# Performance work log

Hardware: AMD Instinct MI355X
Metric: run time of the kernel (lower is better)

## Reference

```python
import jax, jax.numpy as jnp
import numpy as np

# Standard asymmetric NF4 value table (bitsandbytes / flute nf_utils, bits=4, symmetric=False)
NF4_VALUES = np.array([
    -1.0, -0.6961928009986877, -0.5250730514526367, -0.39491748809814453,
    -0.28444138169288635, -0.18477343022823334, -0.09105003625154495, 0.0,
    0.07958029955625534, 0.16093020141124725, 0.2461123913526535,
    0.33791524171829224, 0.44070982933044434, 0.5626170039176941,
    0.7229568362236023, 1.0], dtype=np.float32)
# Pivots are midpoints between consecutive values -> nearest-value bucketing via searchsorted
NF4_PIVOTS = (NF4_VALUES[:-1] + NF4_VALUES[1:]) / 2.0

GROUP_SIZE = 64
IN_FEATURES = 4096
OUT_FEATURES = 4096
BATCH, SEQ = 4, 2048


def setup_inputs() -> dict:
    key = jax.random.key(0)
    k1, k2 = jax.random.split(key)
    inp = jax.random.normal(k1, (BATCH, SEQ, IN_FEATURES), dtype=jnp.float32)
    weight = jax.random.normal(k2, (OUT_FEATURES, IN_FEATURES), dtype=jnp.float32) * 0.02
    # scales initialized exactly as in __init__: per-group absmax of the weight
    scales = jnp.max(jnp.abs(weight.reshape(-1, GROUP_SIZE)), axis=1, keepdims=True)  # [out*in/64, 1]
    return {
        "inp": inp,
        "weight": weight,
        "scales": scales,
        "values": jnp.asarray(NF4_VALUES),
        "pivots": jnp.asarray(NF4_PIVOTS),
    }


def _manual_nf4(weight, scales, values, pivots, group_size):
    # groupwise absmax-normalize, nearest-value lookup via pivot search, dequantize
    w = weight.reshape(-1, group_size)                 # [n_groups, group_size]
    scaled = jnp.clip(w / scales, -1.0, 1.0)
    idx = jnp.searchsorted(pivots, scaled)             # nearest NF4 code
    qweight = values[idx] * scales                     # dequantized bf16-style weight
    return qweight.reshape(weight.shape)


def reference(inp, weight, scales, values, pivots):
    qweight = _manual_nf4(weight, scales, values, pivots, GROUP_SIZE)  # [out, in]
    # F.linear(inp, qweight), bias=None
    return jnp.einsum('bsi,oi->bso', inp, qweight)
```

## Files before the change

kernel.cpp:

```cpp
#include <hip/hip_runtime.h>
#include <hip/hip_bf16.h>
#include <stdint.h>

#define M_DIM 8192
#define N_DIM 4096
#define K_DIM 4096
#define BM 256
#define BN 256
#define BK 64
#define NT (K_DIM / BK)

#define CVT_BLOCKS 8192
#define DQ_BLOCKS  4096

typedef float f32x16 __attribute__((ext_vector_type(16)));
typedef __bf16 bf16x8 __attribute__((ext_vector_type(8)));
typedef short s16x8 __attribute__((ext_vector_type(8)));

template <typename AB>
__device__ __forceinline__ auto mfma_32x32x16(AB a, AB b, f32x16 c, int)
    -> decltype(__builtin_amdgcn_mfma_f32_32x32x16_bf16(a, b, c, 0, 0, 0)) {
  return __builtin_amdgcn_mfma_f32_32x32x16_bf16(a, b, c, 0, 0, 0);
}
template <typename AB>
__device__ __forceinline__ f32x16 mfma_32x32x16(AB a, AB b, f32x16 c, long) {
  return __builtin_amdgcn_mfma_f32_32x32x16_bf16(
      __builtin_bit_cast(s16x8, a), __builtin_bit_cast(s16x8, b), c, 0, 0, 0);
}

__device__ __forceinline__ uint16_t f2b(float f) {
  union { float f; uint32_t u; } v; v.f = f;
  uint32_t u = v.u;
  u += 0x7FFFu + ((u >> 16) & 1u);
  return (uint16_t)(u >> 16);
}

__global__ __launch_bounds__(256) void prep(const float* __restrict__ inp,
                                            uint16_t* __restrict__ A_bf16,
                                            const float* __restrict__ w,
                                            const float* __restrict__ scales,
                                            const float* __restrict__ values,
                                            const float* __restrict__ pivots,
                                            uint16_t* __restrict__ B_bf16) {
  if (blockIdx.x < CVT_BLOCKS) {
    size_t t0 = (size_t)blockIdx.x * 256 + threadIdx.x;
    const float4* pin = (const float4*)inp;
    uint2* pout = (uint2*)A_bf16;
#pragma unroll
    for (int it = 0; it < 4; ++it) {
      size_t i = t0 + (size_t)it * ((size_t)CVT_BLOCKS * 256);
      float4 a = pin[i];
      uint2 o;
      o.x = (uint32_t)f2b(a.x) | ((uint32_t)f2b(a.y) << 16);
      o.y = (uint32_t)f2b(a.z) | ((uint32_t)f2b(a.w) << 16);
      pout[i] = o;
    }
  } else {
    __shared__ float sv[16];
    if (threadIdx.x < 16) sv[threadIdx.x] = values[threadIdx.x];
    float pv[15];
#pragma unroll
    for (int j = 0; j < 15; ++j) pv[j] = pivots[j];
    __syncthreads();
    size_t t0 = (size_t)(blockIdx.x - CVT_BLOCKS) * 256 + threadIdx.x;
    const float4* pw = (const float4*)w;
    uint2* pout = (uint2*)B_bf16;
#pragma unroll
    for (int it = 0; it < 4; ++it) {
      size_t i = t0 + (size_t)it * ((size_t)DQ_BLOCKS * 256);
      float scale = scales[i >> 4];
      float psc[15];
#pragma unroll
      for (int j = 0; j < 15; ++j) psc[j] = pv[j] * scale;
      float4 a = pw[i];
      float e[4] = {a.x, a.y, a.z, a.w};
      uint32_t hw[4];
#pragma unroll
      for (int k = 0; k < 4; ++k) {
        int idx = 0;
#pragma unroll
        for (int j = 0; j < 15; ++j) idx += (psc[j] < e[k]) ? 1 : 0;
        hw[k] = f2b(sv[idx] * scale);
      }
      uint2 o = {hw[0] | (hw[1] << 16), hw[2] | (hw[3] << 16)};
      pout[i] = o;
    }
  }
}


#define GLL(SRC, LOFF)                                                        \
  __builtin_amdgcn_global_load_lds(                                           \
      (__attribute__((address_space(1))) void*)(void*)(SRC),                  \
      (__attribute__((address_space(3))) void*)(smem + (LOFF)), 16, 0, 0)

#define STAGE_A(NB, KH, KEL)                                                  \
  do {                                                                        \
    GLL(Ab + gs0 + (KEL) + (KH) * 32, (NB) * 32768u + (KH) * 16384u + l0);    \
    GLL(Ab + gs1 + (KEL) + (KH) * 32, (NB) * 32768u + (KH) * 16384u + l1);    \
  } while (0)
#define STAGE_B(NB, KH, KEL)                                                  \
  do {                                                                        \
    GLL(Bb + gs0 + (KEL) + (KH) * 32,                                         \
        65536u + (NB) * 32768u + (KH) * 16384u + l0);                         \
    GLL(Bb + gs1 + (KEL) + (KH) * 32,                                         \
        65536u + (NB) * 32768u + (KH) * 16384u + l1);                         \
  } while (0)

#define LGKM6                                                                 \
  do {                                                                        \
    asm volatile("s_waitcnt lgkmcnt(6)" ::: "memory");                        \
    __builtin_amdgcn_sched_barrier(0);                                        \
  } while (0)
#define LGKM0                                                                 \
  do {                                                                        \
    asm volatile("s_waitcnt lgkmcnt(0)" ::: "memory");                        \
    __builtin_amdgcn_sched_barrier(0);                                        \
  } while (0)

#define READ6(A0, A1, A2, A3, B0, B1, CUR, KH, CB)                            \
  do {                                                                        \
    const uint32_t _ab = (CUR) * 32768u + (KH) * 16384u + aoff;               \
    const uint32_t _bb = 65536u + (CUR) * 32768u + (KH) * 16384u + boff;      \
    A0 = *(const bf16x8*)(smem + _ab + (CB));                                 \
    B0 = *(const bf16x8*)(smem + _bb + (CB));                                 \
    B1 = *(const bf16x8*)(smem + _bb + 2048u + (CB));                         \
    A1 = *(const bf16x8*)(smem + _ab + 2048u + (CB));                         \
    A2 = *(const bf16x8*)(smem + _ab + 4096u + (CB));                         \
    A3 = *(const bf16x8*)(smem + _ab + 6144u + (CB));                         \
  } while (0)

#define MM8(A0, A1, A2, A3, B0, B1)                                           \
  do {                                                                        \
    __builtin_amdgcn_s_setprio(1);                                            \
    acc[0][0] = mfma_32x32x16(A0, B0, acc[0][0], 0);                          \
    acc[0][1] = mfma_32x32x16(A0, B1, acc[0][1], 0);                          \
    acc[1][0] = mfma_32x32x16(A1, B0, acc[1][0], 0);                          \
    acc[1][1] = mfma_32x32x16(A1, B1, acc[1][1], 0);                          \
    acc[2][0] = mfma_32x32x16(A2, B0, acc[2][0], 0);                          \
    acc[2][1] = mfma_32x32x16(A2, B1, acc[2][1], 0);                          \
    acc[3][0] = mfma_32x32x16(A3, B0, acc[3][0], 0);                          \
    acc[3][1] = mfma_32x32x16(A3, B1, acc[3][1], 0);                          \
    __builtin_amdgcn_sched_barrier(0);                                        \
    __builtin_amdgcn_s_setprio(0);                                            \
  } while (0)

#define TILE(CUR, NB, KEL)                                                    \
  do {                                                                        \
    bf16x8 xa0, xa1, xa2, xa3, xb0, xb1;                                      \
    bf16x8 ya0, ya1, ya2, ya3, yb0, yb1;                                      \
    READ6(xa0, xa1, xa2, xa3, xb0, xb1, CUR, 0u, cb0);            \
    STAGE_A(NB, 0u, KEL);                                                     \
    STAGE_B(NB, 0u, KEL);                                                     \
    READ6(ya0, ya1, ya2, ya3, yb0, yb1, CUR, 0u, cb1);            \
    LGKM6;                                                 \
    MM8(xa0, xa1, xa2, xa3, xb0, xb1);                                        \
    READ6(xa0, xa1, xa2, xa3, xb0, xb1, CUR, 1u, cb0);            \
    STAGE_A(NB, 1u, KEL);                                                     \
    STAGE_B(NB, 1u, KEL);                                                     \
    LGKM6;                                                 \
    MM8(ya0, ya1, ya2, ya3, yb0, yb1);                                        \
    READ6(ya0, ya1, ya2, ya3, yb0, yb1, CUR, 1u, cb1);            \
    LGKM6;                                                 \
    MM8(xa0, xa1, xa2, xa3, xb0, xb1);                                        \
    LGKM0;                                                 \
    MM8(ya0, ya1, ya2, ya3, yb0, yb1);                                        \
    asm volatile("s_waitcnt vmcnt(0)" ::: "memory");  \
    __builtin_amdgcn_s_barrier();                                             \
    __builtin_amdgcn_sched_barrier(0);                                        \
  } while (0)

__global__ __launch_bounds__(512, 2) void gemm_bt(const uint16_t* __restrict__ A,
                                                  const uint16_t* __restrict__ B,
                                                  float* __restrict__ C) {
  __shared__ char smem[131072];
  const int tid = threadIdx.x;
  const int wave = tid >> 6;
  const int lane = tid & 63;

  const int bid = blockIdx.x;
  const int wg = (bid & 7) * 64 + (bid >> 3);
  const int bm = wg >> 4;
  const int bn = wg & 15;

  const int wm = wave >> 2;
  const int wn = wave & 3;
  const int r31 = lane & 31;
  const int hi = lane >> 5;

  const int swz = ((r31 >> 1) & 3) ^ ((r31 >> 3) & 1);
  const uint32_t cb0 = (uint32_t)(((hi ^ swz) * 16));
  const uint32_t cb1 = (uint32_t)((((2 + hi) ^ swz) * 16));
  const uint32_t aoff = (uint32_t)(wm * 8192 + r31 * 64);
  const uint32_t boff = (uint32_t)(wn * 4096 + r31 * 64);

  const int s0 = wave * 128 + lane;
  const int r0 = s0 >> 2;
  const uint32_t gs0 =
      (uint32_t)r0 * K_DIM +
      (uint32_t)((((s0 & 3) ^ (((r0 >> 1) & 3) ^ ((r0 >> 3) & 1))) * 8));
  const int s1 = s0 + 64;
  const int r1 = s1 >> 2;
  const uint32_t gs1 =
      (uint32_t)r1 * K_DIM +
      (uint32_t)((((s1 & 3) ^ (((r1 >> 1) & 3) ^ ((r1 >> 3) & 1))) * 8));
  const uint32_t l0 = (uint32_t)(wave * 2048);
  const uint32_t l1 = l0 + 1024u;

  const uint16_t* Ab = A + (size_t)bm * BM * K_DIM;
  const uint16_t* Bb = B + (size_t)bn * BN * K_DIM;

  f32x16 acc[4][2] = {};

  STAGE_A(0u, 0u, 0u);
  STAGE_B(0u, 0u, 0u);
  STAGE_A(0u, 1u, 0u);
  STAGE_B(0u, 1u, 0u);
  asm volatile("s_waitcnt vmcnt(0)" ::: "memory");
  __builtin_amdgcn_s_barrier();
  __builtin_amdgcn_sched_barrier(0);

  for (int kt = 0; kt < NT; kt += 2) {
    const uint32_t kel0 = (uint32_t)(kt + 1) * BK;
    const uint32_t kel1 =
        (uint32_t)((kt + 2 < NT) ? (kt + 2) : (NT - 1)) * BK;
    TILE(0u, 1u, kel0);
    TILE(1u, 0u, kel1);
  }

  const int crow0 = bm * BM + wm * 128;
  const int ccol0 = bn * BN + wn * 64 + r31;
#pragma unroll
  for (int i = 0; i < 4; ++i)
#pragma unroll
    for (int j = 0; j < 2; ++j)
#pragma unroll
      for (int reg = 0; reg < 16; ++reg) {
        int row = i * 32 + (reg & 3) + 8 * (reg >> 2) + 4 * hi;
        C[(size_t)(crow0 + row) * N_DIM + ccol0 + j * 32] = acc[i][j][reg];
      }
}

extern "C" void kernel_launch(void* const* d_in, const int* in_sizes, int n_in,
                              void* d_out, int out_size, void* d_ws, size_t ws_size,
                              hipStream_t stream) {
  const float* inp    = (const float*)d_in[0];
  const float* weight = (const float*)d_in[1];
  const float* scales = (const float*)d_in[2];
  const float* values = (const float*)d_in[3];
  const float* pivots = (const float*)d_in[4];
  float* out = (float*)d_out;

  uint16_t* A_bf16 = (uint16_t*)d_ws;
  uint16_t* B_bf16 = A_bf16 + (size_t)M_DIM * K_DIM;

  prep<<<CVT_BLOCKS + DQ_BLOCKS, 256, 0, stream>>>(inp, A_bf16, weight, scales,
                                                   values, pivots, B_bf16);
  gemm_bt<<<dim3(512), 512, 0, stream>>>(A_bf16, B_bf16, out);
}
```

Before: 541.0 us.

## Split GEMM tile into half-K phases with partial vmcnt waits and barriers

Restructures the main loop so each K-half runs as its own phase: it issues all LDS reads, then the global-to-LDS staging for the next buffer, waits on lgkmcnt, barriers, and runs 16 MFMAs at raised priority. The end-of-tile vmcnt(0) drain becomes vmcnt(4), so the next tile's second-half loads can stay in flight across barriers, with a final drain after the loop. The aim is to overlap global loads with compute for longer and to cut full pipeline stalls. In exchange it adds a barrier per phase and gives up the interleaving of LDS reads with MFMAs, and correctness now rests on the partial wait counts matching the actual load order.

After: 530.9 us. About the same (-1.9%).

```diff
diff --git a/kernel.cpp b/kernel.cpp
--- a/kernel.cpp
+++ b/kernel.cpp
@@ -107,17 +107,6 @@
         65536u + (NB) * 32768u + (KH) * 16384u + l1);                         \
   } while (0)
 
-#define LGKM6                                                                 \
-  do {                                                                        \
-    asm volatile("s_waitcnt lgkmcnt(6)" ::: "memory");                        \
-    __builtin_amdgcn_sched_barrier(0);                                        \
-  } while (0)
-#define LGKM0                                                                 \
-  do {                                                                        \
-    asm volatile("s_waitcnt lgkmcnt(0)" ::: "memory");                        \
-    __builtin_amdgcn_sched_barrier(0);                                        \
-  } while (0)
-
 #define READ6(A0, A1, A2, A3, B0, B1, CUR, KH, CB)                            \
   do {                                                                        \
     const uint32_t _ab = (CUR) * 32768u + (KH) * 16384u + aoff;               \
@@ -130,9 +119,8 @@
     A3 = *(const bf16x8*)(smem + _ab + 6144u + (CB));                         \
   } while (0)
 
-#define MM8(A0, A1, A2, A3, B0, B1)                                           \
-  do {                                                                        \
-    __builtin_amdgcn_s_setprio(1);                                            \
+#define MFMA8(A0, A1, A2, A3, B0, B1)                                         \
+  do {                                                                        \
     acc[0][0] = mfma_32x32x16(A0, B0, acc[0][0], 0);                          \
     acc[0][1] = mfma_32x32x16(A0, B1, acc[0][1], 0);                          \
     acc[1][0] = mfma_32x32x16(A1, B0, acc[1][0], 0);                          \
@@ -141,31 +129,26 @@
     acc[2][1] = mfma_32x32x16(A2, B1, acc[2][1], 0);                          \
     acc[3][0] = mfma_32x32x16(A3, B0, acc[3][0], 0);                          \
     acc[3][1] = mfma_32x32x16(A3, B1, acc[3][1], 0);                          \
+  } while (0)
+
+#define PHASE(CUR, NB, KH, KEL)                                               \
+  do {                                                                        \
+    bf16x8 xa0, xa1, xa2, xa3, xb0, xb1;                                      \
+    bf16x8 ya0, ya1, ya2, ya3, yb0, yb1;                                      \
+    READ6(xa0, xa1, xa2, xa3, xb0, xb1, CUR, KH, cb0);      \
+    READ6(ya0, ya1, ya2, ya3, yb0, yb1, CUR, KH, cb1);      \
+    STAGE_A(NB, KH, KEL);                                                     \
+    STAGE_B(NB, KH, KEL);                                                     \
+    asm volatile("s_waitcnt lgkmcnt(8)" ::: "memory");       \
+    __builtin_amdgcn_s_barrier();                                             \
+    asm volatile("s_waitcnt lgkmcnt(0)" ::: "memory");                        \
+    __builtin_amdgcn_sched_barrier(0);                                        \
+    __builtin_amdgcn_s_setprio(1);                                            \
+    MFMA8(xa0, xa1, xa2, xa3, xb0, xb1);                                      \
+    MFMA8(ya0, ya1, ya2, ya3, yb0, yb1);                                      \
     __builtin_amdgcn_sched_barrier(0);                                        \
     __builtin_amdgcn_s_setprio(0);                                            \
-  } while (0)
-
-#define TILE(CUR, NB, KEL)                                                    \
-  do {                                                                        \
-    bf16x8 xa0, xa1, xa2, xa3, xb0, xb1;                                      \
-    bf16x8 ya0, ya1, ya2, ya3, yb0, yb1;                                      \
-    READ6(xa0, xa1, xa2, xa3, xb0, xb1, CUR, 0u, cb0);            \
-    STAGE_A(NB, 0u, KEL);                                                     \
-    STAGE_B(NB, 0u, KEL);                                                     \
-    READ6(ya0, ya1, ya2, ya3, yb0, yb1, CUR, 0u, cb1);            \
-    LGKM6;                                                 \
-    MM8(xa0, xa1, xa2, xa3, xb0, xb1);                                        \
-    READ6(xa0, xa1, xa2, xa3, xb0, xb1, CUR, 1u, cb0);            \
-    STAGE_A(NB, 1u, KEL);                                                     \
-    STAGE_B(NB, 1u, KEL);                                                     \
-    LGKM6;                                                 \
-    MM8(ya0, ya1, ya2, ya3, yb0, yb1);                                        \
-    READ6(ya0, ya1, ya2, ya3, yb0, yb1, CUR, 1u, cb1);            \
-    LGKM6;                                                 \
-    MM8(xa0, xa1, xa2, xa3, xb0, xb1);                                        \
-    LGKM0;                                                 \
-    MM8(ya0, ya1, ya2, ya3, yb0, yb1);                                        \
-    asm volatile("s_waitcnt vmcnt(0)" ::: "memory");  \
+    asm volatile("s_waitcnt vmcnt(4)" ::: "memory");    \
     __builtin_amdgcn_s_barrier();                                             \
     __builtin_amdgcn_sched_barrier(0);                                        \
   } while (0)
@@ -216,7 +199,7 @@
   STAGE_B(0u, 0u, 0u);
   STAGE_A(0u, 1u, 0u);
   STAGE_B(0u, 1u, 0u);
-  asm volatile("s_waitcnt vmcnt(0)" ::: "memory");
+  asm volatile("s_waitcnt vmcnt(4)" ::: "memory");
   __builtin_amdgcn_s_barrier();
   __builtin_amdgcn_sched_barrier(0);
 
@@ -224,9 +207,13 @@
     const uint32_t kel0 = (uint32_t)(kt + 1) * BK;
     const uint32_t kel1 =
         (uint32_t)((kt + 2 < NT) ? (kt + 2) : (NT - 1)) * BK;
-    TILE(0u, 1u, kel0);
-    TILE(1u, 0u, kel1);
+    PHASE(0u, 1u, 0u, kel0);
+    PHASE(0u, 1u, 1u, kel0);
+    PHASE(1u, 0u, 0u, kel1);
+    PHASE(1u, 0u, 1u, kel1);
   }
+
+  asm volatile("s_waitcnt vmcnt(0)" ::: "memory");
 
   const int crow0 = bm * BM + wm * 128;
   const int ccol0 = bn * BN + wn * 64 + r31;
```
